# Optimization experiments

Measured on AMD Instinct MI355X. Metric: run time of the kernel, lower is better.

## Reference

```python
import jax, jax.numpy as jnp
import numpy as np

ALPHA = 1000.0  # Voting(1000) temperature
EPS_NORM = 1e-12
RIDGE = 1e-6


def _edge_index(n):
    # gh(): complete directed graph, edges enumerated i-major, j skipping diagonal.
    ii, jj = np.meshgrid(np.arange(n), np.arange(n), indexing='ij')
    off = ii != jj
    src = ii[off].astype(np.int32)   # G one-hot column = source node
    tgt = jj[off].astype(np.int32)   # H one-hot column = target node
    eid = np.zeros((n, n), dtype=np.int32)
    eid[off] = np.arange(src.size, dtype=np.int32)
    return src, tgt, eid, off


def _l2norm_rows(x):
    return x / jnp.maximum(jnp.linalg.norm(x, axis=1, keepdims=True), EPS_NORM)


def _forward(data1, data2, W, b):
    n1 = data1.shape[0]
    n2 = data2.shape[0]
    src1, tgt1, eid1, off1 = _edge_index(n1)
    src2, tgt2, eid2, off2 = _edge_index(n2)

    # cross-graph embedding update
    Mp0 = data1 @ data2.T                      # [n1, n2]
    m1 = Mp0 @ data2                           # [n1, 512]
    m2 = Mp0.T @ data1                         # [n2, 512]
    lam1 = jax.lax.stop_gradient(
        jnp.linalg.norm(data1, axis=1, keepdims=True)
        / jnp.linalg.norm(m1, axis=1, keepdims=True))
    lam2 = jax.lax.stop_gradient(
        jnp.linalg.norm(data2, axis=1, keepdims=True)
        / jnp.linalg.norm(m2, axis=1, keepdims=True))
    e1 = jax.nn.relu((data1 + lam1 * m1) @ W.T + b)
    e2 = jax.nn.relu((data2 + lam2 * m2) @ W.T + b)
    e1 = _l2norm_rows(e1)
    e2 = _l2norm_rows(e2)

    # edge affinity Me = X2^T Y2 / 2 with X2 = [F@G; F@H] (G/H one-hot => gathers)
    Me = (e1[src1] @ e2[src2].T + e1[tgt1] @ e2[tgt2].T) * 0.5   # [E1, E2]
    Mp = e1 @ e2.T                                               # [n1, n2]

    # Kronecker affinity: M[(i2*n1+i1),(j2*n1+j1)] = Me[eid1[i1,j1], eid2[i2,j2]]
    # (exact value of (a2*K_G) @ K_H^T for complete-graph one-hot incidences)
    g = Me[eid1][:, :, eid2]                                     # [i1, j1, i2, j2]
    mask = off1[:, :, None, None] & off2[None, None, :, :]
    g = jnp.where(mask, g, 0.0)
    Mmat = jnp.transpose(g, (2, 0, 3, 1)).reshape(n1 * n2, n1 * n2)

    Nv = n1 * n2
    kconst = (n1 - 1) * (n2 - 1)
    Q = (kconst + RIDGE) * jnp.eye(Nv, dtype=Mmat.dtype) - Mmat
    Mpp = Mp.T.reshape(Nv)

    # equality constraints of the n1==n2 branch (doubly-stochastic-sum rows),
    # one redundant row dropped so the KKT system is nonsingular
    A1 = jnp.kron(jnp.ones((1, n1), Mmat.dtype), jnp.eye(n2, dtype=Mmat.dtype))
    A2 = jnp.kron(jnp.eye(n1, dtype=Mmat.dtype), jnp.ones((1, n2), Mmat.dtype))
    A = jnp.concatenate([A1, A2], 0)[:-1]
    nc = A.shape[0]

    # QP  min 1/2 z^T Q z - Mpp^T z  s.t. A z = 1  (equality KKT solve;
    # z>=0 handled by the subsequent clamp as in the released pipeline)
    KKT = jnp.block([[Q, A.T], [A, jnp.zeros((nc, nc), Mmat.dtype)]])
    rhs = jnp.concatenate([Mpp, jnp.ones(nc, Mmat.dtype)])
    z = jnp.linalg.solve(KKT, rhs)[:Nv]

    s = z.reshape(n2, n1).T                 # [n1, n2]
    s = jnp.clip(s, 0.0, 1.0)               # relu(s) - relu(s-1)
    s = jax.nn.softmax(ALPHA * s, axis=-1)[None]  # Voting(1000)
    return s


def setup_inputs() -> dict:
    key = jax.random.key(0)
    k1, k2, k3, k4 = jax.random.split(key, 4)
    n, d = 80, 512
    data1 = jax.random.normal(k1, (n, d), dtype=jnp.float32)
    data2 = jax.random.normal(k2, (n, d), dtype=jnp.float32)
    # cross_graph Linear initialized to identity (nn.init.eye_) + tiny jitter
    W = jnp.eye(d, dtype=jnp.float32) + 0.01 * jax.random.normal(k3, (d, d), dtype=jnp.float32)
    b = 0.01 * jax.random.normal(k4, (d,), dtype=jnp.float32)
    return {"data1": data1, "data2": data2, "W": W, "b": b}


def reference(data1, data2, W, b):
    return _forward(data1, data2, W, b)
```

## Files before the change

kernel.cpp:

```cpp
#include <hip/hip_runtime.h>
#include <math.h>

#define N 80
#define D 512
#define NV (N*N)
#define CQ 6241.000001
#define NEU_K 2

__device__ float g_Mp0[N*N];
__device__ float g_WT[D*D];
__device__ float g_e[2][N*D];
__device__ float g_P[NV];

__global__ void k_pre(const float* __restrict__ W,
                      const float* __restrict__ d1, const float* __restrict__ d2) {
    int bid = blockIdx.x;
    int tid = threadIdx.x;
    if (bid < 256) {
        __shared__ float t[32][33];
        int c0 = (bid & 15)*32, k0 = (bid >> 4)*32;
        int tx = tid & 31, ty = tid >> 5;
        #pragma unroll
        for (int j = 0; j < 4; ++j) t[ty+8*j][tx] = W[(size_t)(k0+ty+8*j)*D + c0+tx];
        __syncthreads();
        #pragma unroll
        for (int j = 0; j < 4; ++j) g_WT[(size_t)(c0+ty+8*j)*D + k0+tx] = t[tx][ty+8*j];
    } else {
        int gidx = (bid-256)*256 + tid;
        int v = gidx >> 3, ch = gidx & 7;
        int i = v / N, j = v % N;
        const float4* A = reinterpret_cast<const float4*>(d1 + (size_t)i*D);
        const float4* B = reinterpret_cast<const float4*>(d2 + (size_t)j*D);
        float a0=0,a1=0,a2=0,a3=0;
        #pragma unroll
        for (int t = 0; t < 16; ++t) {
            float4 x = A[ch + 8*t], y = B[ch + 8*t];
            a0 += x.x*y.x; a1 += x.y*y.y;
            a2 += x.z*y.z; a3 += x.w*y.w;
        }
        float s = (a0+a1)+(a2+a3);
        #pragma unroll
        for (int o = 1; o < 8; o <<= 1) s += __shfl_xor(s, o, 64);
        if (ch == 0) g_Mp0[i*N+j] = s;
    }
}

__device__ __forceinline__ float bsum512f(float v, float* w8, int tid) {
    #pragma unroll
    for (int o = 1; o < 64; o <<= 1) v += __shfl_xor(v, o, 64);
    if ((tid & 63) == 0) w8[tid >> 6] = v;
    __syncthreads();
    return ((w8[0]+w8[1])+(w8[2]+w8[3])) + ((w8[4]+w8[5])+(w8[6]+w8[7]));
}

__global__ void __launch_bounds__(512,1) k_mue(const float* __restrict__ d1,
                                               const float* __restrict__ d2,
                                               const float* __restrict__ b) {
    __shared__ float mp[N];
    __shared__ float su[D];
    __shared__ float w8a[8], w8b[8];
    int bid = blockIdx.x;
    int g = bid / N, row = bid % N;
    int tid = threadIdx.x;
    const float* dsrc = g ? d1 : d2;
    const float* dme  = g ? d2 : d1;

    if (tid < N) mp[tid] = g ? g_Mp0[tid*N + row] : g_Mp0[row*N + tid];
    __syncthreads();

    float m0=0,m1=0,m2=0,m3=0,m4=0,m5=0,m6=0,m7=0;
    #pragma unroll 2
    for (int j = 0; j < N; j += 8) {
        m0 += mp[j]   * dsrc[(size_t)j*D     + tid];
        m1 += mp[j+1] * dsrc[(size_t)(j+1)*D + tid];
        m2 += mp[j+2] * dsrc[(size_t)(j+2)*D + tid];
        m3 += mp[j+3] * dsrc[(size_t)(j+3)*D + tid];
        m4 += mp[j+4] * dsrc[(size_t)(j+4)*D + tid];
        m5 += mp[j+5] * dsrc[(size_t)(j+5)*D + tid];
        m6 += mp[j+6] * dsrc[(size_t)(j+6)*D + tid];
        m7 += mp[j+7] * dsrc[(size_t)(j+7)*D + tid];
    }
    float mk = ((m0+m1)+(m2+m3)) + ((m4+m5)+(m6+m7));
    float ak = dme[(size_t)row*D + tid];

    float sa = bsum512f(ak*ak, w8a, tid);
    float sm = bsum512f(mk*mk, w8b, tid);
    float lam = sqrtf(sa) / sqrtf(sm);
    __syncthreads();
    su[tid] = ak + lam*mk;
    __syncthreads();

    const float* wt = g_WT + tid;
    float a0=0,a1=0,a2=0,a3=0,a4=0,a5=0,a6=0,a7=0;
    float b0=0,b1=0,b2=0,b3=0,b4=0,b5=0,b6=0,b7=0;
    #pragma unroll 4
    for (int t = 0; t < 32; ++t) {
        int c = t*16;
        a0 += su[c+0]*wt[(size_t)(c+0)*D];
        a1 += su[c+1]*wt[(size_t)(c+1)*D];
        a2 += su[c+2]*wt[(size_t)(c+2)*D];
        a3 += su[c+3]*wt[(size_t)(c+3)*D];
        a4 += su[c+4]*wt[(size_t)(c+4)*D];
        a5 += su[c+5]*wt[(size_t)(c+5)*D];
        a6 += su[c+6]*wt[(size_t)(c+6)*D];
        a7 += su[c+7]*wt[(size_t)(c+7)*D];
        b0 += su[c+8]*wt[(size_t)(c+8)*D];
        b1 += su[c+9]*wt[(size_t)(c+9)*D];
        b2 += su[c+10]*wt[(size_t)(c+10)*D];
        b3 += su[c+11]*wt[(size_t)(c+11)*D];
        b4 += su[c+12]*wt[(size_t)(c+12)*D];
        b5 += su[c+13]*wt[(size_t)(c+13)*D];
        b6 += su[c+14]*wt[(size_t)(c+14)*D];
        b7 += su[c+15]*wt[(size_t)(c+15)*D];
    }
    float acc = b[tid]
              + (((a0+a1)+(a2+a3)) + ((a4+a5)+(a6+a7)))
              + (((b0+b1)+(b2+b3)) + ((b4+b5)+(b6+b7)));
    float ek = acc > 0.0f ? acc : 0.0f;

    float sn = bsum512f(ek*ek, w8a, tid);
    float nrm = sqrtf(sn); if (nrm < 1e-12f) nrm = 1e-12f;
    g_e[g][(size_t)row*D + tid] = ek / nrm;
}

__global__ void k_p() {
    int gidx = blockIdx.x*256 + threadIdx.x;
    int v = gidx >> 3, ch = gidx & 7;
    int i1 = v % N, i2 = v / N;
    const float4* a  = reinterpret_cast<const float4*>(g_e[0] + (size_t)i1*D);
    const float4* c2 = reinterpret_cast<const float4*>(g_e[1] + (size_t)i2*D);
    float a0=0,a1=0,a2=0,a3=0;
    #pragma unroll
    for (int t = 0; t < 16; ++t) {
        float4 x = a[ch + 8*t], y = c2[ch + 8*t];
        a0 += x.x*y.x; a1 += x.y*y.y;
        a2 += x.z*y.z; a3 += x.w*y.w;
    }
    float s = (a0+a1)+(a2+a3);
    #pragma unroll
    for (int o = 1; o < 8; o <<= 1) s += __shfl_xor(s, o, 64);
    if (ch == 0) g_P[v] = s;
}

__global__ void __launch_bounds__(256,1) k_out(float* __restrict__ out) {
    __shared__ double sv[NV];
    __shared__ double sR[N], sC[N];
    __shared__ double ssc[4];
    __shared__ float  sox[N*(N+1)];
    const double inv80 = 1.0/80.0, inv6400 = 1.0/6400.0, CHI = 1.0/80.0;
    const double invCQ = 1.0/CQ;
    int tid = threadIdx.x;
    double ploc[25], vv[25], x[25];

    #pragma unroll
    for (int j = 0; j < 25; ++j) { int v = tid + 256*j; ploc[j] = (double)g_P[v]; sv[v] = ploc[j]; }
    __syncthreads();

    if (tid < N) {
        double cs = 0.0; const double* dd = sv + tid*N;
        for (int i1 = 0; i1 < N; ++i1) cs += dd[i1];
        sC[tid] = cs;
    } else if (tid < 2*N) {
        int i1 = tid - N; double rr = 0.0;
        for (int i2 = 0; i2 < N; ++i2) rr += sv[i2*N + i1];
        sR[i1] = rr;
    }
    __syncthreads();
    if (tid == 0) { double s = 0.0; for (int i = 0; i < N; ++i) s += sC[i]; ssc[0] = s; }
    __syncthreads();
    double Tp = ssc[0];
    const double SCALE = 6402.0/160.0;
    #pragma unroll
    for (int j = 0; j < 25; ++j) {
        int v = tid + 256*j; int i1 = v % N, i2 = v / N;
        double rv = SCALE*(ploc[j] - sR[i1]*inv80 - sC[i2]*inv80 + Tp*inv6400);
        vv[j] = rv;
        x[j]  = rv*invCQ;
    }
    __syncthreads();

    for (int k = 0; k < NEU_K; ++k) {
        #pragma unroll
        for (int j = 0; j < 25; ++j) { int v = tid + 256*j; sv[v] = ploc[j]*vv[j]; }
        __syncthreads();
        if (tid < N) {
            double cs = 0.0; const double* dd = sv + tid*N;
            for (int i1 = 0; i1 < N; ++i1) cs += dd[i1];
            sC[tid] = cs;
        } else if (tid < 2*N) {
            int i1 = tid - N; double rr = 0.0;
            for (int i2 = 0; i2 < N; ++i2) rr += sv[i2*N + i1];
            sR[i1] = rr;
        }
        __syncthreads();
        if (tid == 0) { double s = 0.0; for (int i = 0; i < N; ++i) s += sC[i]; ssc[1] = s; }
        __syncthreads();
        double Ty = ssc[1];
        #pragma unroll
        for (int j = 0; j < 25; ++j) {
            int v = tid + 256*j; int i1 = v % N, i2 = v / N;
            double mv = ploc[j]*vv[j] - sR[i1]*inv80 - sC[i2]*inv80 + Ty*inv6400;
            vv[j] = mv*invCQ;
            x[j] += vv[j]*invCQ;
        }
        __syncthreads();
    }

    #pragma unroll
    for (int j = 0; j < 25; ++j) {
        int v = tid + 256*j;
        double z = CHI + x[j];
        sv[v] = z < 0.0 ? 0.0 : (z > 1.0 ? 1.0 : z);
    }
    __syncthreads();
    if (tid < N) {
        double mx = -1e300;
        for (int i2 = 0; i2 < N; ++i2) mx = fmax(mx, sv[i2*N + tid]);
        sR[tid] = mx;
    }
    __syncthreads();
    #pragma unroll
    for (int j = 0; j < 25; ++j) {
        int v = tid + 256*j; int i1 = v % N;
        sv[v] = exp(1000.0*(sv[v] - sR[i1]));
    }
    __syncthreads();
    if (tid < N) {
        double s = 0.0;
        for (int i2 = 0; i2 < N; ++i2) s += sv[i2*N + tid];
        sC[tid] = 1.0 / s;
    }
    __syncthreads();
    #pragma unroll
    for (int j = 0; j < 25; ++j) {
        int v = tid + 256*j; int i1 = v % N, i2 = v / N;
        sox[i1*(N+1) + i2] = (float)(sv[v] * sC[i1]);
    }
    __syncthreads();
    for (int w = tid; w < NV; w += 256) {
        int i1 = w / N, i2 = w % N;
        out[w] = sox[i1*(N+1) + i2];
    }
}

extern "C" void kernel_launch(void* const* d_in, const int* in_sizes, int n_in,
                              void* d_out, int out_size, void* d_ws, size_t ws_size,
                              hipStream_t stream) {
    const float* d1 = (const float*)d_in[0];
    const float* d2 = (const float*)d_in[1];
    const float* W  = (const float*)d_in[2];
    const float* b  = (const float*)d_in[3];
    float* out = (float*)d_out;

    k_pre<<<dim3(456), dim3(256), 0, stream>>>(W, d1, d2);
    k_mue<<<dim3(160), dim3(512), 0, stream>>>(d1, d2, b);
    k_p  <<<dim3(200), dim3(256), 0, stream>>>();
    k_out<<<dim3(1),   dim3(256), 0, stream>>>(out);
}
```

Baseline: 63.19 us.

## Process two rows per block in k_mue to reuse W and data loads

```diff
diff --git a/kernel.cpp b/kernel.cpp
--- a/kernel.cpp
+++ b/kernel.cpp
@@ -56,71 +56,77 @@
 __global__ void __launch_bounds__(512,1) k_mue(const float* __restrict__ d1,
                                                const float* __restrict__ d2,
                                                const float* __restrict__ b) {
-    __shared__ float mp[N];
-    __shared__ float su[D];
+    __shared__ float mp0[N], mp1[N];
+    __shared__ float su0[D], su1[D];
     __shared__ float w8a[8], w8b[8];
     int bid = blockIdx.x;
-    int g = bid / N, row = bid % N;
+    int g = bid / 40;
+    int r0 = (bid % 40) * 2;
     int tid = threadIdx.x;
     const float* dsrc = g ? d1 : d2;
     const float* dme  = g ? d2 : d1;
 
-    if (tid < N) mp[tid] = g ? g_Mp0[tid*N + row] : g_Mp0[row*N + tid];
-    __syncthreads();
-
-    float m0=0,m1=0,m2=0,m3=0,m4=0,m5=0,m6=0,m7=0;
-    #pragma unroll 2
-    for (int j = 0; j < N; j += 8) {
-        m0 += mp[j]   * dsrc[(size_t)j*D     + tid];
-        m1 += mp[j+1] * dsrc[(size_t)(j+1)*D + tid];
-        m2 += mp[j+2] * dsrc[(size_t)(j+2)*D + tid];
-        m3 += mp[j+3] * dsrc[(size_t)(j+3)*D + tid];
-        m4 += mp[j+4] * dsrc[(size_t)(j+4)*D + tid];
-        m5 += mp[j+5] * dsrc[(size_t)(j+5)*D + tid];
-        m6 += mp[j+6] * dsrc[(size_t)(j+6)*D + tid];
-        m7 += mp[j+7] * dsrc[(size_t)(j+7)*D + tid];
-    }
-    float mk = ((m0+m1)+(m2+m3)) + ((m4+m5)+(m6+m7));
-    float ak = dme[(size_t)row*D + tid];
-
-    float sa = bsum512f(ak*ak, w8a, tid);
-    float sm = bsum512f(mk*mk, w8b, tid);
-    float lam = sqrtf(sa) / sqrtf(sm);
-    __syncthreads();
-    su[tid] = ak + lam*mk;
+    if (tid < N) {
+        mp0[tid] = g ? g_Mp0[tid*N + r0] : g_Mp0[r0*N + tid];
+    } else if (tid < 2*N) {
+        int j = tid - N;
+        mp1[j] = g ? g_Mp0[j*N + (r0+1)] : g_Mp0[(r0+1)*N + j];
+    }
+    __syncthreads();
+
+    float ma0=0,ma1=0,ma2=0,ma3=0, mb0=0,mb1=0,mb2=0,mb3=0;
+    #pragma unroll 4
+    for (int j = 0; j < N; j += 4) {
+        float w0 = dsrc[(size_t)j*D     + tid];
+        float w1 = dsrc[(size_t)(j+1)*D + tid];
+        float w2 = dsrc[(size_t)(j+2)*D + tid];
+        float w3 = dsrc[(size_t)(j+3)*D + tid];
+        ma0 += mp0[j]*w0; ma1 += mp0[j+1]*w1; ma2 += mp0[j+2]*w2; ma3 += mp0[j+3]*w3;
+        mb0 += mp1[j]*w0; mb1 += mp1[j+1]*w1; mb2 += mp1[j+2]*w2; mb3 += mp1[j+3]*w3;
+    }
+    float mk0 = (ma0+ma1)+(ma2+ma3);
+    float mk1 = (mb0+mb1)+(mb2+mb3);
+    float ak0 = dme[(size_t)r0*D + tid];
+    float ak1 = dme[(size_t)(r0+1)*D + tid];
+
+    float sa0 = bsum512f(ak0*ak0, w8a, tid);
+    float sm0 = bsum512f(mk0*mk0, w8b, tid);
+    __syncthreads();
+    float sa1 = bsum512f(ak1*ak1, w8a, tid);
+    float sm1 = bsum512f(mk1*mk1, w8b, tid);
+    float lam0 = sqrtf(sa0) / sqrtf(sm0);
+    float lam1 = sqrtf(sa1) / sqrtf(sm1);
+    __syncthreads();
+    su0[tid] = ak0 + lam0*mk0;
+    su1[tid] = ak1 + lam1*mk1;
     __syncthreads();
 
     const float* wt = g_WT + tid;
-    float a0=0,a1=0,a2=0,a3=0,a4=0,a5=0,a6=0,a7=0;
-    float b0=0,b1=0,b2=0,b3=0,b4=0,b5=0,b6=0,b7=0;
-    #pragma unroll 4
+    float A[16], B[16];
+    #pragma unroll
+    for (int q = 0; q < 16; ++q) { A[q] = 0.0f; B[q] = 0.0f; }
     for (int t = 0; t < 32; ++t) {
         int c = t*16;
-        a0 += su[c+0]*wt[(size_t)(c+0)*D];
-        a1 += su[c+1]*wt[(size_t)(c+1)*D];
-        a2 += su[c+2]*wt[(size_t)(c+2)*D];
-        a3 += su[c+3]*wt[(size_t)(c+3)*D];
-        a4 += su[c+4]*wt[(size_t)(c+4)*D];
-        a5 += su[c+5]*wt[(size_t)(c+5)*D];
-        a6 += su[c+6]*wt[(size_t)(c+6)*D];
-        a7 += su[c+7]*wt[(size_t)(c+7)*D];
-        b0 += su[c+8]*wt[(size_t)(c+8)*D];
-        b1 += su[c+9]*wt[(size_t)(c+9)*D];
-        b2 += su[c+10]*wt[(size_t)(c+10)*D];
-        b3 += su[c+11]*wt[(size_t)(c+11)*D];
-        b4 += su[c+12]*wt[(size_t)(c+12)*D];
-        b5 += su[c+13]*wt[(size_t)(c+13)*D];
-        b6 += su[c+14]*wt[(size_t)(c+14)*D];
-        b7 += su[c+15]*wt[(size_t)(c+15)*D];
-    }
-    float acc = b[tid]
-              + (((a0+a1)+(a2+a3)) + ((a4+a5)+(a6+a7)))
-              + (((b0+b1)+(b2+b3)) + ((b4+b5)+(b6+b7)));
-    float ek = acc > 0.0f ? acc : 0.0f;
-
-    float sn = bsum512f(ek*ek, w8a, tid);
-    float nrm = sqrtf(sn); if (nrm < 1e-12f) nrm = 1e-12f;
-    g_e[g][(size_t)row*D + tid] = ek / nrm;
+        #pragma unroll
+        for (int q = 0; q < 16; ++q) {
+            float w = wt[(size_t)(c+q)*D];
+            A[q] += su0[c+q]*w;
+            B[q] += su1[c+q]*w;
+        }
+    }
+    float accA = 0.0f, accB = 0.0f;
+    #pragma unroll
+    for (int q = 0; q < 16; ++q) { accA += A[q]; accB += B[q]; }
+    float bk = b[tid];
+    float ek0 = accA + bk; ek0 = ek0 > 0.0f ? ek0 : 0.0f;
+    float ek1 = accB + bk; ek1 = ek1 > 0.0f ? ek1 : 0.0f;
+
+    float sn0 = bsum512f(ek0*ek0, w8a, tid);
+    float sn1 = bsum512f(ek1*ek1, w8b, tid);
+    float n0 = sqrtf(sn0); if (n0 < 1e-12f) n0 = 1e-12f;
+    float n1 = sqrtf(sn1); if (n1 < 1e-12f) n1 = 1e-12f;
+    g_e[g][(size_t)r0*D     + tid] = ek0 / n0;
+    g_e[g][(size_t)(r0+1)*D + tid] = ek1 / n1;
 }
 
 __global__ void k_p() {
@@ -253,7 +259,7 @@
     float* out = (float*)d_out;
 
     k_pre<<<dim3(456), dim3(256), 0, stream>>>(W, d1, d2);
-    k_mue<<<dim3(160), dim3(512), 0, stream>>>(d1, d2, b);
+    k_mue<<<dim3(80),  dim3(512), 0, stream>>>(d1, d2, b);
     k_p  <<<dim3(200), dim3(256), 0, stream>>>();
     k_out<<<dim3(1),   dim3(256), 0, stream>>>(out);
 }
```

Measured after the change: 75.51 us. +19.5%, slower.
